# Kernel optimization log

Hardware: AMD Instinct MI355X
Metric: run time of the kernel (lower is better)

## Reference

```python
import jax, jax.numpy as jnp
import numpy as np

DIM = 1024
HEADS = 16
HEAD_DIM = 64
INNER = HEADS * HEAD_DIM  # 1024
B, N = 4, 2048
EPS = 1e-5


def setup_inputs() -> dict:
    key = jax.random.key(0)
    ks = jax.random.split(key, 5)
    x = jax.random.normal(ks[0], (B, N, DIM), dtype=jnp.float32)
    w_qkv = jax.random.normal(ks[1], (DIM, 3 * INNER), dtype=jnp.float32) * (DIM ** -0.5)
    w_out = jax.random.normal(ks[2], (INNER, DIM), dtype=jnp.float32) * (INNER ** -0.5)
    b_out = jax.random.normal(ks[3], (DIM,), dtype=jnp.float32) * 0.01
    ln_gamma = jnp.ones((DIM,), dtype=jnp.float32)
    ln_beta = jnp.zeros((DIM,), dtype=jnp.float32)
    return {"x": x, "w_qkv": w_qkv, "w_out": w_out, "b_out": b_out,
            "ln_gamma": ln_gamma, "ln_beta": ln_beta}


def reference(x, w_qkv, w_out, b_out, ln_gamma, ln_beta):
    scale = HEAD_DIM ** -0.5
    qkv = x @ w_qkv  # [b, n, 3*inner]
    q, k, v = jnp.split(qkv, 3, axis=-1)
    q = q * scale
    # [b, n, h*d] -> [b, h, n, d]
    def to_heads(t):
        b, n, _ = t.shape
        return t.reshape(b, n, HEADS, HEAD_DIM).transpose(0, 2, 1, 3)
    q, k, v = to_heads(q), to_heads(k), to_heads(v)
    scores = jnp.einsum('bhid,bhjd->bhij', q, k)
    attn = jax.nn.softmax(scores, axis=-1)  # max-subtraction (detached) is internal
    out = jnp.einsum('bhij,bhjd->bhid', attn, v)
    out = out.transpose(0, 2, 1, 3).reshape(x.shape[0], x.shape[1], INNER)
    out = out @ w_out + b_out
    # LayerNorm over last dim
    mu = out.mean(axis=-1, keepdims=True)
    var = out.var(axis=-1, keepdims=True)
    out = (out - mu) * jax.lax.rsqrt(var + EPS)
    return out * ln_gamma + ln_beta
```

## Files before the change

kernel.cpp:

```cpp
#include <hip/hip_runtime.h>


typedef __bf16 bf16;
typedef __bf16 bf16x4 __attribute__((ext_vector_type(4)));
typedef __bf16 bf16x8 __attribute__((ext_vector_type(8)));
typedef float f32x4 __attribute__((ext_vector_type(4)));
typedef unsigned int u32x4 __attribute__((ext_vector_type(4)));

#define QSCALE 0.125f

#define GLOAD_LDS16(gp, lp)                                                   \
  __builtin_amdgcn_global_load_lds(                                           \
      (const __attribute__((address_space(1))) unsigned int*)(const void*)(gp), \
      (__attribute__((address_space(3))) unsigned int*)(void*)(lp), 16, 0, 0)

__device__ __forceinline__ unsigned pack2(float lo, float hi) {
  union { __bf16 b; unsigned short u; } a, c;
  a.b = (__bf16)lo; c.b = (__bf16)hi;
  return (unsigned)a.u | ((unsigned)c.u << 16);
}

__global__ __launch_bounds__(256) void cvt_k(const float* __restrict__ in,
                                             bf16* __restrict__ out) {
  const size_t i = ((size_t)blockIdx.x * 256 + threadIdx.x) * 8;
  float4 a = *(const float4*)(in + i);
  float4 b = *(const float4*)(in + i + 4);
  bf16x8 o = {(bf16)a.x, (bf16)a.y, (bf16)a.z, (bf16)a.w,
              (bf16)b.x, (bf16)b.y, (bf16)b.z, (bf16)b.w};
  *(bf16x8*)(out + i) = o;
}

__global__ __launch_bounds__(256) void transpose_k(const float* __restrict__ in,
                                                   bf16* __restrict__ out,
                                                   int Kd, int Nd) {
  __shared__ bf16 t[32][36];
  const int n0 = blockIdx.x * 32, k0 = blockIdx.y * 32;
  const int r = threadIdx.x >> 3, c4 = (threadIdx.x & 7) * 4;
  float4 v = *(const float4*)(in + (size_t)(k0 + r) * Nd + n0 + c4);
  t[c4 + 0][r] = (bf16)v.x; t[c4 + 1][r] = (bf16)v.y;
  t[c4 + 2][r] = (bf16)v.z; t[c4 + 3][r] = (bf16)v.w;
  __syncthreads();
  bf16x4 o = *(const bf16x4*)&t[r][c4];
  *(bf16x4*)(out + (size_t)(n0 + r) * Kd + k0 + c4) = o;
}

template <bool QKV>
__global__ __launch_bounds__(256) void gemm2(const bf16* __restrict__ A,
                                             const bf16* __restrict__ Bt,
                                             bf16* __restrict__ C,
                                             bf16* __restrict__ Vt) {
  __shared__ bf16 As[128][32];
  __shared__ bf16 Bs[128][32];
  const int tid = threadIdx.x;
  const int l = tid & 63, w = tid >> 6;
  const int g = l >> 4, q = l & 15;
  const int wm = w >> 1, wn = w & 1;
  const int m0 = blockIdx.x * 128, n0 = blockIdx.y * 128;
  const int lr = l >> 2, lc = (l & 3) * 8;

  f32x4 acc[4][4] = {};

  for (int k0 = 0; k0 < 1024; k0 += 32) {
    __syncthreads();
#pragma unroll
    for (int i = 0; i < 2; i++) {
      const int c = w + i * 4;
      GLOAD_LDS16(A + (size_t)(m0 + c * 16 + lr) * 1024 + k0 + lc, &As[c * 16][0]);
      GLOAD_LDS16(Bt + (size_t)(n0 + c * 16 + lr) * 1024 + k0 + lc, &Bs[c * 16][0]);
    }
    __syncthreads();

    bf16x8 af[4], bfr[4];
#pragma unroll
    for (int mi = 0; mi < 4; mi++)
      af[mi] = *(const bf16x8*)&As[wm * 64 + mi * 16 + q][g * 8];
#pragma unroll
    for (int ni = 0; ni < 4; ni++)
      bfr[ni] = *(const bf16x8*)&Bs[wn * 64 + ni * 16 + q][g * 8];
#pragma unroll
    for (int mi = 0; mi < 4; mi++)
#pragma unroll
      for (int ni = 0; ni < 4; ni++)
        acc[mi][ni] = __builtin_amdgcn_mfma_f32_16x16x32_bf16(af[mi], bfr[ni], acc[mi][ni], 0, 0, 0);
  }

  if (QKV && n0 >= 2048) {
#pragma unroll
    for (int mi = 0; mi < 4; mi++)
#pragma unroll
      for (int ni = 0; ni < 4; ni++) {
        const int vcol = n0 - 2048 + wn * 64 + ni * 16 + q;
        const int h = vcol >> 6, d = vcol & 63;
        const int t0 = m0 + wm * 64 + mi * 16 + g * 4;
        const int b = t0 >> 11, n = t0 & 2047;
        bf16x4 o = {(bf16)acc[mi][ni][0], (bf16)acc[mi][ni][1],
                    (bf16)acc[mi][ni][2], (bf16)acc[mi][ni][3]};
        *(bf16x4*)(Vt + ((size_t)(b * 16 + h) * 64 + d) * 2048 + n) = o;
      }
  } else {
    const int ldc = QKV ? 2048 : 1024;
    const float s = (QKV && n0 < 1024) ? QSCALE : 1.0f;
#pragma unroll
    for (int mi = 0; mi < 4; mi++)
#pragma unroll
      for (int ni = 0; ni < 4; ni++) {
        const int col = n0 + wn * 64 + ni * 16 + q;
#pragma unroll
        for (int r = 0; r < 4; r++) {
          const int row = m0 + wm * 64 + mi * 16 + g * 4 + r;
          C[(size_t)row * ldc + col] = (bf16)(acc[mi][ni][r] * s);
        }
      }
  }
}

__global__ __launch_bounds__(512) void attn_k(const bf16* __restrict__ qk,
                                              const bf16* __restrict__ vt,
                                              bf16* __restrict__ aout) {
  __shared__ bf16 Ks[2][64][64];
  __shared__ bf16 Vs[2][64][64];
  const int tid = threadIdx.x;
  const int l = tid & 63, w = tid >> 6;
  const int g = l >> 4, q = l & 15, q7 = q & 7;
  const int h = blockIdx.y, b = blockIdx.z;
  const int q0 = blockIdx.x * 128 + w * 16;

  const bf16* Kg = qk + (size_t)(b * 2048) * 2048 + 1024 + h * 64;
  const bf16* Vg = vt + ((size_t)(b * 16 + h) * 64) * 2048;

  bf16x8 qf[2];
  {
    const bf16* Qr = qk + (size_t)(b * 2048 + q0 + q) * 2048 + h * 64 + g * 8;
    qf[0] = *(const bf16x8*)Qr;
    qf[1] = *(const bf16x8*)(Qr + 32);
  }

  const int r0 = tid >> 3, sp0 = ((tid & 7) ^ (r0 & 7)) * 8;
  const int ub = (tid >> 6) << 9;
#define STAGE_KV(buf, kt)                                                      \
  do {                                                                         \
    GLOAD_LDS16(Kg + (size_t)((kt) + r0) * 2048 + sp0, &Ks[buf][0][0] + ub);   \
    GLOAD_LDS16(Vg + (size_t)r0 * 2048 + (kt) + sp0, &Vs[buf][0][0] + ub);     \
  } while (0)

  float m = -1e30f, lsum = 0.f;
  f32x4 oacc[4] = {};

  STAGE_KV(0, 0);
  __syncthreads();
  int cur = 0;

  for (int kt = 0; kt < 2048; kt += 64) {
    if (kt + 64 < 2048) STAGE_KV(cur ^ 1, kt + 64);

    const char* Kb = (const char*)&Ks[cur][0][0];
    const char* Vb = (const char*)&Vs[cur][0][0];
    const int cb = ((g ^ q7) << 4);

    f32x4 st[4];
    __builtin_amdgcn_s_setprio(1);
#pragma unroll
    for (int t = 0; t < 4; t++) {
      const int rb = (t * 16 + q) * 128;
      bf16x8 kf0 = *(const bf16x8*)(Kb + rb + cb);
      bf16x8 kf1 = *(const bf16x8*)(Kb + rb + (cb ^ 64));
      f32x4 z = {0.f, 0.f, 0.f, 0.f};
      z = __builtin_amdgcn_mfma_f32_16x16x32_bf16(kf0, qf[0], z, 0, 0, 0);
      st[t] = __builtin_amdgcn_mfma_f32_16x16x32_bf16(kf1, qf[1], z, 0, 0, 0);
    }
    __builtin_amdgcn_s_setprio(0);
    bf16x8 vf[4][2];
#pragma unroll
    for (int dc = 0; dc < 4; dc++) {
      const int rb = (dc * 16 + q) * 128;
      vf[dc][0] = *(const bf16x8*)(Vb + rb + cb);
      vf[dc][1] = *(const bf16x8*)(Vb + rb + (cb ^ 64));
    }

    float tmax = st[0][0];
#pragma unroll
    for (int t = 0; t < 4; t++)
#pragma unroll
      for (int r = 0; r < 4; r++) tmax = fmaxf(tmax, st[t][r]);
    tmax = fmaxf(tmax, __shfl_xor(tmax, 16));
    tmax = fmaxf(tmax, __shfl_xor(tmax, 32));
    float corr = 1.0f;
    if (__ballot(tmax > m)) {
      const float mnew = fmaxf(m, tmax);
      corr = __expf(m - mnew);
      m = mnew;
#pragma unroll
      for (int dc = 0; dc < 4; dc++)
#pragma unroll
        for (int r = 0; r < 4; r++) oacc[dc][r] *= corr;
    }
    float p[4][4];
    float tsum = 0.f;
#pragma unroll
    for (int t = 0; t < 4; t++)
#pragma unroll
      for (int r = 0; r < 4; r++) { p[t][r] = __expf(st[t][r] - m); tsum += p[t][r]; }
    tsum += __shfl_xor(tsum, 16);
    tsum += __shfl_xor(tsum, 32);
    lsum = lsum * corr + tsum;

    unsigned pk[4][2];
#pragma unroll
    for (int t = 0; t < 4; t++) {
      pk[t][0] = pack2(p[t][0], p[t][1]);
      pk[t][1] = pack2(p[t][2], p[t][3]);
    }
    u32x4 bwA, bwB;
#pragma unroll
    for (int wd = 0; wd < 4; wd++) {
      const int src = q + 16 * ((g & 1) * 2 + (wd >> 1));
      const unsigned loA = (unsigned)__shfl((int)pk[0][wd & 1], src);
      const unsigned hiA = (unsigned)__shfl((int)pk[1][wd & 1], src);
      const unsigned loB = (unsigned)__shfl((int)pk[2][wd & 1], src);
      const unsigned hiB = (unsigned)__shfl((int)pk[3][wd & 1], src);
      bwA[wd] = (g < 2) ? loA : hiA;
      bwB[wd] = (g < 2) ? loB : hiB;
    }
    const bf16x8 pfA = __builtin_bit_cast(bf16x8, bwA);
    const bf16x8 pfB = __builtin_bit_cast(bf16x8, bwB);

    __builtin_amdgcn_s_setprio(1);
#pragma unroll
    for (int dc = 0; dc < 4; dc++) {
      oacc[dc] = __builtin_amdgcn_mfma_f32_16x16x32_bf16(vf[dc][0], pfA, oacc[dc], 0, 0, 0);
      oacc[dc] = __builtin_amdgcn_mfma_f32_16x16x32_bf16(vf[dc][1], pfB, oacc[dc], 0, 0, 0);
    }
    __builtin_amdgcn_s_setprio(0);

    __syncthreads();
    cur ^= 1;
  }

  const float inv = 1.f / lsum;
  bf16* orow = aout + (size_t)(b * 2048 + q0 + q) * 1024 + h * 64;
#pragma unroll
  for (int dc = 0; dc < 4; dc++) {
    bf16x4 o = {(bf16)(oacc[dc][0] * inv), (bf16)(oacc[dc][1] * inv),
                (bf16)(oacc[dc][2] * inv), (bf16)(oacc[dc][3] * inv)};
    *(bf16x4*)(orow + dc * 16 + g * 4) = o;
  }
#undef STAGE_KV
}

__global__ __launch_bounds__(256) void ln_k(const bf16* __restrict__ proj,
                                            const float* __restrict__ bo,
                                            const float* __restrict__ gam,
                                            const float* __restrict__ bet,
                                            float* __restrict__ out) {
  const int row = blockIdx.x, tid = threadIdx.x;
  const int l = tid & 63, w = tid >> 6;
  bf16x4 pv = *(const bf16x4*)(proj + (size_t)row * 1024 + tid * 4);
  float4 bv = *(const float4*)(bo + tid * 4);
  float v0 = (float)pv[0] + bv.x, v1 = (float)pv[1] + bv.y;
  float v2 = (float)pv[2] + bv.z, v3 = (float)pv[3] + bv.w;
  float s = v0 + v1 + v2 + v3;
  float ss = v0 * v0 + v1 * v1 + v2 * v2 + v3 * v3;
#pragma unroll
  for (int off = 32; off > 0; off >>= 1) {
    s += __shfl_xor(s, off);
    ss += __shfl_xor(ss, off);
  }
  __shared__ float red[8];
  if (l == 0) { red[w] = s; red[w + 4] = ss; }
  __syncthreads();
  const float S = red[0] + red[1] + red[2] + red[3];
  const float SS = red[4] + red[5] + red[6] + red[7];
  const float mean = S * (1.f / 1024.f);
  const float var = SS * (1.f / 1024.f) - mean * mean;
  const float rs = rsqrtf(var + 1e-5f);
  float4 gv = *(const float4*)(gam + tid * 4);
  float4 btv = *(const float4*)(bet + tid * 4);
  float4 o;
  o.x = (v0 - mean) * rs * gv.x + btv.x;
  o.y = (v1 - mean) * rs * gv.y + btv.y;
  o.z = (v2 - mean) * rs * gv.z + btv.z;
  o.w = (v3 - mean) * rs * gv.w + btv.w;
  *(float4*)(out + (size_t)row * 1024 + tid * 4) = o;
}

extern "C" void kernel_launch(void* const* d_in, const int* in_sizes, int n_in,
                              void* d_out, int out_size, void* d_ws, size_t ws_size,
                              hipStream_t stream) {
  const float* x      = (const float*)d_in[0];
  const float* w_qkv  = (const float*)d_in[1];
  const float* w_out  = (const float*)d_in[2];
  const float* b_out  = (const float*)d_in[3];
  const float* gamma  = (const float*)d_in[4];
  const float* beta   = (const float*)d_in[5];
  float* out = (float*)d_out;

  char* ws = (char*)d_ws;
  bf16* xbf   = (bf16*)(ws);
  bf16* wqkvT = (bf16*)(ws + 16777216);
  bf16* woutT = (bf16*)(ws + 23068672);
  bf16* qkbuf = (bf16*)(ws + 25165824);
  bf16* vt    = (bf16*)(ws + 58720256);
  bf16* aout  = xbf;
  bf16* proj  = vt;

  dim3 blk(256);
  cvt_k<<<4096, blk, 0, stream>>>(x, xbf);
  transpose_k<<<dim3(96, 32), blk, 0, stream>>>(w_qkv, wqkvT, 1024, 3072);
  transpose_k<<<dim3(32, 32), blk, 0, stream>>>(w_out, woutT, 1024, 1024);
  gemm2<true><<<dim3(64, 24), blk, 0, stream>>>(xbf, wqkvT, qkbuf, vt);
  attn_k<<<dim3(16, 16, 4), dim3(512), 0, stream>>>(qkbuf, vt, aout);
  gemm2<false><<<dim3(64, 8), blk, 0, stream>>>(aout, woutT, proj, nullptr);
  ln_k<<<8192, blk, 0, stream>>>(proj, b_out, gamma, beta, out);
}
```

Before: 246.3 us.

## Switch attention to 32x32x16 MFMA with 4 waves of 32 query rows

The attention kernel now uses 32x32x16 bf16 MFMA instead of 16x16x32, with each wave covering 32 query rows, so the block drops from 8 to 4 waves over the same 128 rows. The P fragment is rebuilt with permlane32_swap instead of the generic shuffle sequence, and row max/sum reductions use a single permlane32 swap. The bigger MFMA tile is meant to reuse K/V fragments more per LDS read and to cut shuffle overhead. In exchange there are fewer waves per block to hide latency, and the 16-wide accumulators raise register pressure.

Measured after the change: 253.8 us. 1.03x slower.

```diff
diff --git a/kernel.cpp b/kernel.cpp
--- a/kernel.cpp
+++ b/kernel.cpp
@@ -5,6 +5,8 @@
 typedef __bf16 bf16x4 __attribute__((ext_vector_type(4)));
 typedef __bf16 bf16x8 __attribute__((ext_vector_type(8)));
 typedef float f32x4 __attribute__((ext_vector_type(4)));
+typedef float f32x16 __attribute__((ext_vector_type(16)));
+typedef unsigned int u32x2 __attribute__((ext_vector_type(2)));
 typedef unsigned int u32x4 __attribute__((ext_vector_type(4)));
 
 #define QSCALE 0.125f
@@ -114,37 +116,41 @@
   }
 }
 
-__global__ __launch_bounds__(512) void attn_k(const bf16* __restrict__ qk,
+__global__ __launch_bounds__(256) void attn_k(const bf16* __restrict__ qk,
                                               const bf16* __restrict__ vt,
                                               bf16* __restrict__ aout) {
   __shared__ bf16 Ks[2][64][64];
   __shared__ bf16 Vs[2][64][64];
   const int tid = threadIdx.x;
   const int l = tid & 63, w = tid >> 6;
-  const int g = l >> 4, q = l & 15, q7 = q & 7;
+  const int q = l & 31, hi = l >> 5, q7 = q & 7;
   const int h = blockIdx.y, b = blockIdx.z;
-  const int q0 = blockIdx.x * 128 + w * 16;
+  const int qbase = blockIdx.x * 128 + w * 32;
 
   const bf16* Kg = qk + (size_t)(b * 2048) * 2048 + 1024 + h * 64;
   const bf16* Vg = vt + ((size_t)(b * 16 + h) * 64) * 2048;
 
-  bf16x8 qf[2];
+  bf16x8 qf[4];
   {
-    const bf16* Qr = qk + (size_t)(b * 2048 + q0 + q) * 2048 + h * 64 + g * 8;
-    qf[0] = *(const bf16x8*)Qr;
-    qf[1] = *(const bf16x8*)(Qr + 32);
+    const bf16* Qr = qk + (size_t)(b * 2048 + qbase + q) * 2048 + h * 64 + hi * 8;
+#pragma unroll
+    for (int i = 0; i < 4; i++) qf[i] = *(const bf16x8*)(Qr + i * 16);
   }
 
   const int r0 = tid >> 3, sp0 = ((tid & 7) ^ (r0 & 7)) * 8;
   const int ub = (tid >> 6) << 9;
-#define STAGE_KV(buf, kt)                                                      \
-  do {                                                                         \
-    GLOAD_LDS16(Kg + (size_t)((kt) + r0) * 2048 + sp0, &Ks[buf][0][0] + ub);   \
-    GLOAD_LDS16(Vg + (size_t)r0 * 2048 + (kt) + sp0, &Vs[buf][0][0] + ub);     \
+#define STAGE_KV(buf, kt)                                                       \
+  do {                                                                          \
+    GLOAD_LDS16(Kg + (size_t)((kt) + r0) * 2048 + sp0, &Ks[buf][0][0] + ub);    \
+    GLOAD_LDS16(Vg + (size_t)r0 * 2048 + (kt) + sp0, &Vs[buf][0][0] + ub);      \
+    GLOAD_LDS16(Kg + (size_t)((kt) + 32 + r0) * 2048 + sp0,                     \
+                &Ks[buf][0][0] + 2048 + ub);                                    \
+    GLOAD_LDS16(Vg + (size_t)(32 + r0) * 2048 + (kt) + sp0,                     \
+                &Vs[buf][0][0] + 2048 + ub);                                    \
   } while (0)
 
   float m = -1e30f, lsum = 0.f;
-  f32x4 oacc[4] = {};
+  f32x16 oacc[2] = {};
 
   STAGE_KV(0, 0);
   __syncthreads();
@@ -155,81 +161,86 @@
 
     const char* Kb = (const char*)&Ks[cur][0][0];
     const char* Vb = (const char*)&Vs[cur][0][0];
-    const int cb = ((g ^ q7) << 4);
-
-    f32x4 st[4];
+
+    f32x16 st[2];
     __builtin_amdgcn_s_setprio(1);
 #pragma unroll
-    for (int t = 0; t < 4; t++) {
-      const int rb = (t * 16 + q) * 128;
-      bf16x8 kf0 = *(const bf16x8*)(Kb + rb + cb);
-      bf16x8 kf1 = *(const bf16x8*)(Kb + rb + (cb ^ 64));
-      f32x4 z = {0.f, 0.f, 0.f, 0.f};
-      z = __builtin_amdgcn_mfma_f32_16x16x32_bf16(kf0, qf[0], z, 0, 0, 0);
-      st[t] = __builtin_amdgcn_mfma_f32_16x16x32_bf16(kf1, qf[1], z, 0, 0, 0);
+    for (int s = 0; s < 2; s++) {
+      f32x16 acc = {};
+#pragma unroll
+      for (int i = 0; i < 4; i++) {
+        bf16x8 kf = *(const bf16x8*)(Kb + (s * 32 + q) * 128 + (((2 * i + hi) ^ q7) << 4));
+        acc = __builtin_amdgcn_mfma_f32_32x32x16_bf16(kf, qf[i], acc, 0, 0, 0);
+      }
+      st[s] = acc;
     }
     __builtin_amdgcn_s_setprio(0);
-    bf16x8 vf[4][2];
-#pragma unroll
-    for (int dc = 0; dc < 4; dc++) {
-      const int rb = (dc * 16 + q) * 128;
-      vf[dc][0] = *(const bf16x8*)(Vb + rb + cb);
-      vf[dc][1] = *(const bf16x8*)(Vb + rb + (cb ^ 64));
-    }
-
-    float tmax = st[0][0];
-#pragma unroll
-    for (int t = 0; t < 4; t++)
-#pragma unroll
-      for (int r = 0; r < 4; r++) tmax = fmaxf(tmax, st[t][r]);
-    tmax = fmaxf(tmax, __shfl_xor(tmax, 16));
-    tmax = fmaxf(tmax, __shfl_xor(tmax, 32));
+
+    bf16x8 vfr[2][4];
+#pragma unroll
+    for (int dblk = 0; dblk < 2; dblk++)
+#pragma unroll
+      for (int t = 0; t < 4; t++)
+        vfr[dblk][t] = *(const bf16x8*)(Vb + (dblk * 32 + q) * 128 + (((2 * t + hi) ^ q7) << 4));
+
+    float mx[8];
+#pragma unroll
+    for (int r = 0; r < 8; r++)
+      mx[r] = fmaxf(fmaxf(st[0][r], st[0][r + 8]), fmaxf(st[1][r], st[1][r + 8]));
+#pragma unroll
+    for (int o = 4; o > 0; o >>= 1)
+#pragma unroll
+      for (int r = 0; r < o; r++) mx[r] = fmaxf(mx[r], mx[r + o]);
+    float tmax;
+    {
+      u32x2 t2 = __builtin_amdgcn_permlane32_swap(__float_as_uint(mx[0]),
+                                                  __float_as_uint(mx[0]), false, false);
+      tmax = fmaxf(__uint_as_float(t2[0]), __uint_as_float(t2[1]));
+    }
     float corr = 1.0f;
     if (__ballot(tmax > m)) {
       const float mnew = fmaxf(m, tmax);
       corr = __expf(m - mnew);
       m = mnew;
 #pragma unroll
-      for (int dc = 0; dc < 4; dc++)
-#pragma unroll
-        for (int r = 0; r < 4; r++) oacc[dc][r] *= corr;
-    }
-    float p[4][4];
+      for (int dblk = 0; dblk < 2; dblk++)
+#pragma unroll
+        for (int r = 0; r < 16; r++) oacc[dblk][r] *= corr;
+    }
     float tsum = 0.f;
 #pragma unroll
-    for (int t = 0; t < 4; t++)
-#pragma unroll
-      for (int r = 0; r < 4; r++) { p[t][r] = __expf(st[t][r] - m); tsum += p[t][r]; }
-    tsum += __shfl_xor(tsum, 16);
-    tsum += __shfl_xor(tsum, 32);
+    for (int s = 0; s < 2; s++)
+#pragma unroll
+      for (int r = 0; r < 16; r++) { st[s][r] = __expf(st[s][r] - m); tsum += st[s][r]; }
+    {
+      u32x2 t2 = __builtin_amdgcn_permlane32_swap(__float_as_uint(tsum),
+                                                  __float_as_uint(tsum), false, false);
+      tsum = __uint_as_float(t2[0]) + __uint_as_float(t2[1]);
+    }
     lsum = lsum * corr + tsum;
 
-    unsigned pk[4][2];
-#pragma unroll
-    for (int t = 0; t < 4; t++) {
-      pk[t][0] = pack2(p[t][0], p[t][1]);
-      pk[t][1] = pack2(p[t][2], p[t][3]);
-    }
-    u32x4 bwA, bwB;
-#pragma unroll
-    for (int wd = 0; wd < 4; wd++) {
-      const int src = q + 16 * ((g & 1) * 2 + (wd >> 1));
-      const unsigned loA = (unsigned)__shfl((int)pk[0][wd & 1], src);
-      const unsigned hiA = (unsigned)__shfl((int)pk[1][wd & 1], src);
-      const unsigned loB = (unsigned)__shfl((int)pk[2][wd & 1], src);
-      const unsigned hiB = (unsigned)__shfl((int)pk[3][wd & 1], src);
-      bwA[wd] = (g < 2) ? loA : hiA;
-      bwB[wd] = (g < 2) ? loB : hiB;
-    }
-    const bf16x8 pfA = __builtin_bit_cast(bf16x8, bwA);
-    const bf16x8 pfB = __builtin_bit_cast(bf16x8, bwB);
+    bf16x8 pfrag[4];
+#pragma unroll
+    for (int s = 0; s < 2; s++)
+#pragma unroll
+      for (int ks = 0; ks < 2; ks++) {
+        const unsigned a0 = pack2(st[s][8 * ks + 0], st[s][8 * ks + 1]);
+        const unsigned a1 = pack2(st[s][8 * ks + 2], st[s][8 * ks + 3]);
+        const unsigned b0 = pack2(st[s][8 * ks + 4], st[s][8 * ks + 5]);
+        const unsigned b1 = pack2(st[s][8 * ks + 6], st[s][8 * ks + 7]);
+        u32x2 w0 = __builtin_amdgcn_permlane32_swap(a0, b0, false, false);
+        u32x2 w1 = __builtin_amdgcn_permlane32_swap(a1, b1, false, false);
+        u32x4 bw = {w0[0], w1[0], w0[1], w1[1]};
+        pfrag[2 * s + ks] = __builtin_bit_cast(bf16x8, bw);
+      }
 
     __builtin_amdgcn_s_setprio(1);
 #pragma unroll
-    for (int dc = 0; dc < 4; dc++) {
-      oacc[dc] = __builtin_amdgcn_mfma_f32_16x16x32_bf16(vf[dc][0], pfA, oacc[dc], 0, 0, 0);
-      oacc[dc] = __builtin_amdgcn_mfma_f32_16x16x32_bf16(vf[dc][1], pfB, oacc[dc], 0, 0, 0);
-    }
+    for (int dblk = 0; dblk < 2; dblk++)
+#pragma unroll
+      for (int t = 0; t < 4; t++)
+        oacc[dblk] = __builtin_amdgcn_mfma_f32_32x32x16_bf16(vfr[dblk][t], pfrag[t],
+                                                             oacc[dblk], 0, 0, 0);
     __builtin_amdgcn_s_setprio(0);
 
     __syncthreads();
@@ -237,13 +248,15 @@
   }
 
   const float inv = 1.f / lsum;
-  bf16* orow = aout + (size_t)(b * 2048 + q0 + q) * 1024 + h * 64;
-#pragma unroll
-  for (int dc = 0; dc < 4; dc++) {
-    bf16x4 o = {(bf16)(oacc[dc][0] * inv), (bf16)(oacc[dc][1] * inv),
-                (bf16)(oacc[dc][2] * inv), (bf16)(oacc[dc][3] * inv)};
-    *(bf16x4*)(orow + dc * 16 + g * 4) = o;
-  }
+  bf16* orow = aout + (size_t)(b * 2048 + qbase + q) * 1024 + h * 64 + hi * 4;
+#pragma unroll
+  for (int dblk = 0; dblk < 2; dblk++)
+#pragma unroll
+    for (int rg = 0; rg < 4; rg++) {
+      bf16x4 o = {(bf16)(oacc[dblk][4 * rg + 0] * inv), (bf16)(oacc[dblk][4 * rg + 1] * inv),
+                  (bf16)(oacc[dblk][4 * rg + 2] * inv), (bf16)(oacc[dblk][4 * rg + 3] * inv)};
+      *(bf16x4*)(orow + dblk * 32 + rg * 8) = o;
+    }
 #undef STAGE_KV
 }
 
@@ -308,7 +321,7 @@
   transpose_k<<<dim3(96, 32), blk, 0, stream>>>(w_qkv, wqkvT, 1024, 3072);
   transpose_k<<<dim3(32, 32), blk, 0, stream>>>(w_out, woutT, 1024, 1024);
   gemm2<true><<<dim3(64, 24), blk, 0, stream>>>(xbf, wqkvT, qkbuf, vt);
-  attn_k<<<dim3(16, 16, 4), dim3(512), 0, stream>>>(qkbuf, vt, aout);
+  attn_k<<<dim3(16, 16, 4), blk, 0, stream>>>(qkbuf, vt, aout);
   gemm2<false><<<dim3(64, 8), blk, 0, stream>>>(aout, woutT, proj, nullptr);
   ln_k<<<8192, blk, 0, stream>>>(proj, b_out, gamma, beta, out);
 }
```
